# Performance work log

Hardware: AMD Instinct MI355X
Metric: run time of the kernel (lower is better)

## Reference

```python
import jax, jax.numpy as jnp
import numpy as np

EPS = 1e-8

def div_small(a, b):
    b_safe = b * (b > EPS) + (b <= EPS) * EPS
    return a / b_safe

def cos_full(q1h, q2h, w):
    # q1h [b,s1,h], q2h [b,s1_or_1,h], w [P,h] -> [b,s1,P]
    a = q1h[:, :, None, :] * w          # [b,s1,P,h]
    c = q2h[:, :, None, :] * w          # [b,s1|1,P,h]
    num = jnp.sum(a * c, axis=-1)
    den = jnp.maximum(jnp.linalg.norm(a, axis=-1) * jnp.linalg.norm(c, axis=-1), EPS)
    return num / den

def cos_maxpool(q1h, q2h, w):
    # q1h [b,s1,h], q2h [b,s2,h], w [P,h] -> max over s2 of cosine -> [b,s1,P]
    a = q1h[:, :, None, :] * w          # [b,s1,P,h]
    c = q2h[:, :, None, :] * w          # [b,s2,P,h]
    num = jnp.einsum('biph,bjph->bijp', a, c)            # [b,s1,s2,P]
    na = jnp.linalg.norm(a, axis=-1)                     # [b,s1,P]
    nc = jnp.linalg.norm(c, axis=-1)                     # [b,s2,P]
    den = jnp.maximum(na[:, :, None, :] * nc[:, None, :, :], EPS)
    return jnp.max(num / den, axis=2)

def attention(q1, q2):
    # cosine-similarity matrix [b,s1,s2]
    n1 = jnp.linalg.norm(q1, axis=2, keepdims=True)      # [b,s1,1]
    n2 = jnp.linalg.norm(q2, axis=2, keepdims=True)      # [b,s2,1]
    num = jnp.einsum('bih,bjh->bij', q1, q2)
    return div_small(num, n1 * jnp.swapaxes(n2, 1, 2))

def setup_inputs() -> dict:
    key = jax.random.key(0)
    k1, k2, kw = jax.random.split(key, 3)
    q1_batch = jax.random.normal(k1, (16, 128, 512), dtype=jnp.float32)
    q2_batch = jax.random.normal(k2, (16, 128, 512), dtype=jnp.float32)
    W = jax.random.normal(kw, (8, 16, 256), dtype=jnp.float32)
    return {"q1_batch": q1_batch, "q2_batch": q2_batch, "W": W}

def reference(q1_batch, q2_batch, W):
    h = q1_batch.shape[-1] // 2
    q1_fw, q1_bw = q1_batch[..., :h], q1_batch[..., h:]
    q2_fw, q2_bw = q2_batch[..., :h], q2_batch[..., h:]

    # 1) full matching against last (fw) / first (bw) q2 state
    full_fw = cos_full(q1_fw, q2_fw[:, -1:, :], W[0])
    full_bw = cos_full(q1_bw, q2_bw[:, :1, :], W[1])

    # 2) max-pool matching over all q2 positions
    max_fw = cos_maxpool(q1_fw, q2_fw, W[2])
    max_bw = cos_maxpool(q1_bw, q2_bw, W[3])

    # 3) attentive matching
    att_fw = attention(q1_fw, q2_fw)                     # [b,s1,s2]
    att_bw = attention(q1_bw, q2_bw)
    at_q2_fw = att_fw[..., None] * q2_fw[:, None, :, :]  # [b,s1,s2,h]
    at_q2_bw = att_bw[..., None] * q2_bw[:, None, :, :]
    mean_fw = div_small(at_q2_fw.sum(axis=2), att_fw.sum(axis=2, keepdims=True))
    # NOTE: denominator intentionally uses att_fw (bug preserved from source)
    mean_bw = div_small(at_q2_bw.sum(axis=2), att_fw.sum(axis=2, keepdims=True))
    attn_fw = cos_full(q1_fw, mean_fw, W[4])
    attn_bw = cos_full(q1_bw, mean_bw, W[5])

    # 4) max-attentive matching
    max_at_fw = at_q2_fw.max(axis=2)                     # [b,s1,h]
    max_at_bw = at_q2_bw.max(axis=2)
    maxattn_fw = cos_full(q1_fw, max_at_fw, W[6])
    maxattn_bw = cos_full(q1_bw, max_at_bw, W[7])

    return jnp.concatenate(
        [full_fw, full_bw, max_fw, max_bw, attn_fw, attn_bw, maxattn_fw, maxattn_bw],
        axis=-1)
```

## Files before the change

kernel.cpp:

```cpp
#include <hip/hip_runtime.h>
#include <hip/hip_bf16.h>

#define B 16
#define L 128
#define H 256
#define H2 512
#define P 16
#define EPSF 1e-8f
#define LDSTR 72

typedef __attribute__((ext_vector_type(8))) short short8;
typedef __attribute__((ext_vector_type(4))) short short4v;
typedef __attribute__((ext_vector_type(4))) float f32x4;

__device__ __forceinline__ short f2bf(float x) {
    unsigned u = __builtin_bit_cast(unsigned, x);
    u += 0x7fffu + ((u >> 16) & 1u);
    return (short)(u >> 16);
}
__device__ __forceinline__ float bf2f(short s) {
    unsigned u = ((unsigned)(unsigned short)s) << 16;
    return __builtin_bit_cast(float, u);
}
__device__ __forceinline__ short8 pack8(float4 x, float4 y) {
    short8 s;
    s[0] = f2bf(x.x); s[1] = f2bf(x.y); s[2] = f2bf(x.z); s[3] = f2bf(x.w);
    s[4] = f2bf(y.x); s[5] = f2bf(y.y); s[6] = f2bf(y.z); s[7] = f2bf(y.w);
    return s;
}
__device__ __forceinline__ float dot4(float4 v) {
    return v.x * v.x + v.y * v.y + v.z * v.z + v.w * v.w;
}
__device__ __forceinline__ float4 mul4(float4 a, float4 b) {
    return make_float4(a.x * b.x, a.y * b.y, a.z * b.z, a.w * b.w);
}

__global__ void __launch_bounds__(64) k_att_v3(
        const float* __restrict__ q1, const float* __restrict__ q2,
        float* __restrict__ att_fw, float* __restrict__ att_bw,
        float* __restrict__ attsum) {
    int bx = blockIdx.x;
    int b = bx >> 1, dir = bx & 1;
    int m0 = blockIdx.y * 16, n0 = blockIdx.z * 16;
    int l = threadIdx.x, q = l >> 4, coll = l & 15;
    size_t bL = (size_t)b * L;

    const float* arow = q1 + (bL + m0 + coll) * H2 + dir * H;
    const float* brow = q2 + (bL + n0 + coll) * H2 + dir * H;

    f32x4 acc = (f32x4){0.f, 0.f, 0.f, 0.f};
    float na = 0.f, nc = 0.f;
#pragma unroll
    for (int ks = 0; ks < 8; ks++) {
        int koff = ks * 32 + q * 8;
        float4 a0 = *(const float4*)(arow + koff);
        float4 a1 = *(const float4*)(arow + koff + 4);
        float4 b0 = *(const float4*)(brow + koff);
        float4 b1 = *(const float4*)(brow + koff + 4);
        na += dot4(a0) + dot4(a1);
        nc += dot4(b0) + dot4(b1);
        short8 af = pack8(a0, a1);
        short8 bf = pack8(b0, b1);
        acc = __builtin_amdgcn_mfma_f32_16x16x32_bf16(af, bf, acc, 0, 0, 0);
    }
    na += __shfl_xor(na, 16); na += __shfl_xor(na, 32);
    nc += __shfl_xor(nc, 16); nc += __shfl_xor(nc, 32);
    float na_s = sqrtf(na), nc_s = sqrtf(nc);

    float* attout = dir ? att_bw : att_fw;
    float rsum[4];
#pragma unroll
    for (int r = 0; r < 4; r++) {
        float nar = __shfl(na_s, (l & 48) + q * 4 + r);
        float den = nar * nc_s;
        den = den > EPSF ? den : EPSF;
        float a = acc[r] / den;
        attout[(bL + m0 + q * 4 + r) * L + n0 + coll] = a;
        rsum[r] = a;
    }
    if (dir == 0) {
#pragma unroll
        for (int off = 1; off < 16; off <<= 1)
#pragma unroll
            for (int r = 0; r < 4; r++)
                rsum[r] += __shfl_xor(rsum[r], off, 16);
        if (coll == 0)
#pragma unroll
            for (int r = 0; r < 4; r++)
                atomicAdd(&attsum[bL + m0 + q * 4 + r], rsum[r]);
    }
}

__global__ void __launch_bounds__(256) k_meanmax_v3(
        const float* __restrict__ q2,
        const float* __restrict__ att_fw, const float* __restrict__ att_bw,
        const float* __restrict__ attsum,
        float* __restrict__ mean_fw, float* __restrict__ mean_bw,
        float* __restrict__ maxat_fw, float* __restrict__ maxat_bw) {
    int bd = blockIdx.x;
    int b = bd >> 1, dir = bd & 1;
    int i0 = blockIdx.y * 4;
    int t = threadIdx.x;
    int wave = t >> 6, l = t & 63;
    size_t bL = (size_t)b * L;

    __shared__ float at[4][L];
    __shared__ float Ss[4];
    __shared__ f32x4 red[4][64][4];

    const float* att = dir ? att_bw : att_fw;
    for (int v = t; v < 4 * L; v += 256)
        at[v >> 7][v & 127] = att[(bL + i0 + (v >> 7)) * L + (v & 127)];
    if (t < 4) {
        float s = attsum[bL + i0 + t];
        Ss[t] = s > EPSF ? s : EPSF;
    }
    __syncthreads();

    f32x4 sum[4], mx[4];
#pragma unroll
    for (int r = 0; r < 4; r++) {
        sum[r] = (f32x4){0.f, 0.f, 0.f, 0.f};
        mx[r] = (f32x4){-INFINITY, -INFINITY, -INFINITY, -INFINITY};
    }
    const float* q2b = q2 + bL * H2 + dir * H;
    for (int jj = 0; jj < 32; jj++) {
        int j = wave * 32 + jj;
        float4 c = *(const float4*)(q2b + (size_t)j * H2 + l * 4);
#pragma unroll
        for (int r = 0; r < 4; r++) {
            float w = at[r][j];
            f32x4 v = { w * c.x, w * c.y, w * c.z, w * c.w };
            sum[r] += v;
            mx[r][0] = fmaxf(mx[r][0], v[0]);
            mx[r][1] = fmaxf(mx[r][1], v[1]);
            mx[r][2] = fmaxf(mx[r][2], v[2]);
            mx[r][3] = fmaxf(mx[r][3], v[3]);
        }
    }
    float* meanout = dir ? mean_bw : mean_fw;
    float* maxout = dir ? maxat_bw : maxat_fw;
    for (int rr = 0; rr < 2; rr++) {
        __syncthreads();
        red[wave][l][0] = sum[rr * 2];
        red[wave][l][1] = mx[rr * 2];
        red[wave][l][2] = sum[rr * 2 + 1];
        red[wave][l][3] = mx[rr * 2 + 1];
        __syncthreads();
        if (t < 128) {
            int r2 = t >> 6;
            int lane = t & 63;
            f32x4 s = red[0][lane][r2 * 2];
            f32x4 m = red[0][lane][r2 * 2 + 1];
            for (int w = 1; w < 4; w++) {
                s += red[w][lane][r2 * 2];
                f32x4 m2 = red[w][lane][r2 * 2 + 1];
                m[0] = fmaxf(m[0], m2[0]);
                m[1] = fmaxf(m[1], m2[1]);
                m[2] = fmaxf(m[2], m2[2]);
                m[3] = fmaxf(m[3], m2[3]);
            }
            int row = i0 + rr * 2 + r2;
            float inv = 1.f / Ss[rr * 2 + r2];
            size_t o = (bL + row) * H + lane * 4;
            *(f32x4*)(meanout + o) = s * inv;
            *(f32x4*)(maxout + o) = m;
        }
    }
}

__global__ void __launch_bounds__(256) k_cosfull_v3(
        const float* __restrict__ q1, const float* __restrict__ q2,
        const float* __restrict__ mean_fw, const float* __restrict__ mean_bw,
        const float* __restrict__ maxat_fw, const float* __restrict__ maxat_bw,
        const float* __restrict__ W, float* __restrict__ out) {
    int bg = blockIdx.x;
    int b = bg >> 4;
    int i0 = (bg & 15) * 8;
    int piece = blockIdx.y;
    int t = threadIdx.x;
    int p = t >> 4, l = t & 15;
    size_t bL = (size_t)b * L;

    int widx, colb, dir, cstride;
    const float* cptr;
    switch (piece) {
        case 0: widx = 0; colb = 0;   dir = 0; cptr = q2 + (bL + L - 1) * H2;  cstride = 0; break;
        case 1: widx = 1; colb = 16;  dir = 1; cptr = q2 + bL * H2 + H;        cstride = 0; break;
        case 2: widx = 4; colb = 64;  dir = 0; cptr = mean_fw + bL * H;        cstride = H; break;
        case 3: widx = 5; colb = 80;  dir = 1; cptr = mean_bw + bL * H;        cstride = H; break;
        case 4: widx = 6; colb = 96;  dir = 0; cptr = maxat_fw + bL * H;       cstride = H; break;
        default: widx = 7; colb = 112; dir = 1; cptr = maxat_bw + bL * H;      cstride = H; break;
    }
    const float* wrow = W + ((size_t)widx * P + p) * H;
    float wsq[16];
#pragma unroll
    for (int k = 0; k < 16; k++) {
        float wv = wrow[l + 16 * k];
        wsq[k] = wv * wv;
    }
    for (int ii = 0; ii < 8; ii++) {
        int i = i0 + ii;
        const float* r1 = q1 + (bL + i) * H2 + dir * H;
        const float* crow = cptr + (size_t)i * cstride;
        float num = 0, na = 0, nc = 0;
#pragma unroll
        for (int k = 0; k < 16; k++) {
            int h = l + 16 * k;
            float a = r1[h];
            float c = crow[h];
            num += a * c * wsq[k];
            na  += a * a * wsq[k];
            nc  += c * c * wsq[k];
        }
        for (int off = 8; off; off >>= 1) {
            num += __shfl_down(num, off, 16);
            na  += __shfl_down(na,  off, 16);
            nc  += __shfl_down(nc,  off, 16);
        }
        if (l == 0) {
            float den = sqrtf(na) * sqrtf(nc);
            den = den > EPSF ? den : EPSF;
            out[(bL + i) * 128 + colb + p] = num / den;
        }
    }
}

__global__ void __launch_bounds__(256) k_maxpool_v2(
        const float* __restrict__ q1, const float* __restrict__ q2,
        const float* __restrict__ W, float* __restrict__ out) {
    int bd = blockIdx.x;
    int b = bd >> 1, dir = bd & 1;
    int p = blockIdx.y;
    int t = threadIdx.x;
    int wave = t >> 6, l = t & 63;
    int q = l >> 4, coll = l & 15;
    int m0 = blockIdx.z * 64 + wave * 16;
    size_t bL = (size_t)b * L;

    __shared__ short Bs[128 * LDSTR];
    __shared__ float wf[H];
    __shared__ float ncs[128];

    if (t < 64)
        *(float4*)(wf + t * 4) =
            *(const float4*)(W + ((size_t)(2 + dir) * P + p) * H + t * 4);
    __syncthreads();

    f32x4 acc[8];
#pragma unroll
    for (int nt = 0; nt < 8; nt++) acc[nt] = (f32x4){0.f, 0.f, 0.f, 0.f};
    float ncp = 0.f, nap = 0.f;

    int brow = t >> 1, bc0 = (t & 1) * 32;
    const float* q1b = q1 + bL * H2 + dir * H;
    const float* q2b = q2 + bL * H2 + dir * H;
    const float* arow = q1b + (size_t)(m0 + coll) * H2;
    const float* brp = q2b + (size_t)brow * H2;

    for (int kt = 0; kt < 4; kt++) {
        int k0 = kt * 64;
#pragma unroll
        for (int cc = 0; cc < 8; cc++) {
            float4 v = *(const float4*)(brp + k0 + bc0 + cc * 4);
            float4 wv4 = *(const float4*)(wf + k0 + bc0 + cc * 4);
            float4 x = mul4(v, wv4);
            short4v s = { f2bf(x.x), f2bf(x.y), f2bf(x.z), f2bf(x.w) };
            *(short4v*)(Bs + brow * LDSTR + bc0 + cc * 4) = s;
            float f0 = bf2f(s[0]), f1 = bf2f(s[1]), f2v = bf2f(s[2]), f3 = bf2f(s[3]);
            ncp += f0 * f0 + f1 * f1 + f2v * f2v + f3 * f3;
        }
        __syncthreads();
#pragma unroll
        for (int ks = 0; ks < 2; ks++) {
            int koff = ks * 32 + q * 8;
            float4 a0 = *(const float4*)(arow + k0 + koff);
            float4 a1 = *(const float4*)(arow + k0 + koff + 4);
            float4 w0 = *(const float4*)(wf + k0 + koff);
            float4 w1 = *(const float4*)(wf + k0 + koff + 4);
            float4 e0 = mul4(a0, w0), e1 = mul4(a1, w1);
            short8 af = pack8(e0, e1);
#pragma unroll
            for (int j = 0; j < 8; j++) {
                float f = bf2f(af[j]);
                nap += f * f;
            }
#pragma unroll
            for (int nt = 0; nt < 8; nt++) {
                short8 bf = *(const short8*)(Bs + (nt * 16 + coll) * LDSTR + koff);
                acc[nt] = __builtin_amdgcn_mfma_f32_16x16x32_bf16(af, bf, acc[nt], 0, 0, 0);
            }
        }
        __syncthreads();
    }
    ncp += __shfl_xor(ncp, 1);
    if ((t & 1) == 0) ncs[brow] = sqrtf(ncp);
    nap += __shfl_xor(nap, 16);
    nap += __shfl_xor(nap, 32);
    float na_s = sqrtf(nap);
    __syncthreads();

    float nar[4];
#pragma unroll
    for (int r = 0; r < 4; r++)
        nar[r] = __shfl(na_s, (l & 48) + q * 4 + r);
    float rmax[4] = {-INFINITY, -INFINITY, -INFINITY, -INFINITY};
#pragma unroll
    for (int nt = 0; nt < 8; nt++) {
        float ncv = ncs[nt * 16 + coll];
#pragma unroll
        for (int r = 0; r < 4; r++) {
            float den = fmaxf(nar[r] * ncv, EPSF);
            rmax[r] = fmaxf(rmax[r], acc[nt][r] / den);
        }
    }
#pragma unroll
    for (int off = 1; off < 16; off <<= 1)
#pragma unroll
        for (int r = 0; r < 4; r++)
            rmax[r] = fmaxf(rmax[r], __shfl_xor(rmax[r], off, 16));
    if (coll == 0)
#pragma unroll
        for (int r = 0; r < 4; r++)
            out[(bL + m0 + q * 4 + r) * 128 + 32 + dir * 16 + p] = rmax[r];
}

extern "C" void kernel_launch(void* const* d_in, const int* in_sizes, int n_in,
                              void* d_out, int out_size, void* d_ws, size_t ws_size,
                              hipStream_t stream) {
    const float* q1 = (const float*)d_in[0];
    const float* q2 = (const float*)d_in[1];
    const float* W  = (const float*)d_in[2];
    float* out = (float*)d_out;

    float* ws = (float*)d_ws;
    float* attsum = ws;
    float* att_fw = attsum + B * L;
    float* att_bw = att_fw + (size_t)B * L * L;
    float* mean_fw = att_bw + (size_t)B * L * L;
    float* mean_bw = mean_fw + (size_t)B * L * H;
    float* maxat_fw = mean_bw + (size_t)B * L * H;
    float* maxat_bw = maxat_fw + (size_t)B * L * H;

    hipMemsetAsync(attsum, 0, B * L * sizeof(float), stream);
    k_maxpool_v2<<<dim3(B * 2, P, 2), 256, 0, stream>>>(q1, q2, W, out);
    k_att_v3<<<dim3(B * 2, 8, 8), 64, 0, stream>>>(q1, q2, att_fw, att_bw, attsum);
    k_meanmax_v3<<<dim3(B * 2, 32), 256, 0, stream>>>(q2, att_fw, att_bw, attsum,
                                                      mean_fw, mean_bw, maxat_fw, maxat_bw);
    k_cosfull_v3<<<dim3(B * 16, 6), 256, 0, stream>>>(q1, q2, mean_fw, mean_bw,
                                                      maxat_fw, maxat_bw, W, out);
}
```

Measured before the change: 132.9 us.

## Add prep kernel for bf16 inputs and norms, restructure att and maxpool kernels

Adds a prep kernel that converts q1/q2 to bf16 and precomputes row norms and per-perspective weighted norms, so the attention and maxpool kernels no longer recompute them. The attention kernel now stages a 16-row A tile and all 128 B rows in LDS, with four waves per block. It reduces the row sums in shared memory and writes them directly instead of using atomics. The maxpool kernel loads the full K range into LDS once instead of looping over K tiles, and cosfull uses vectorized float4 loads. The cost is an extra launch, which redundantly computes weighted norms for 16 perspectives per row, plus extra workspace traffic.

```diff
diff --git a/kernel.cpp b/kernel.cpp
--- a/kernel.cpp
+++ b/kernel.cpp
@@ -7,7 +7,7 @@
 #define H2 512
 #define P 16
 #define EPSF 1e-8f
-#define LDSTR 72
+#define LDSTR2 264
 
 typedef __attribute__((ext_vector_type(8))) short short8;
 typedef __attribute__((ext_vector_type(4))) short short4v;
@@ -35,48 +35,119 @@
     return make_float4(a.x * b.x, a.y * b.y, a.z * b.z, a.w * b.w);
 }
 
-__global__ void __launch_bounds__(64) k_att_v3(
+__global__ void __launch_bounds__(64) k_prep(
         const float* __restrict__ q1, const float* __restrict__ q2,
+        const float* __restrict__ W,
+        short* __restrict__ q1b, short* __restrict__ q2b,
+        float* __restrict__ nex,
+        float* __restrict__ nW) {
+    int row = blockIdx.x;
+    int src = blockIdx.y;
+    int l = threadIdx.x;
+    const float* base = (src ? q2 : q1) + (size_t)row * H2;
+    short* qb = (src ? q2b : q1b) + (size_t)row * H2;
+
+    float4 xf = *(const float4*)(base + l * 4);
+    float4 xb = *(const float4*)(base + H + l * 4);
+    short4v sf = { f2bf(xf.x), f2bf(xf.y), f2bf(xf.z), f2bf(xf.w) };
+    short4v sb = { f2bf(xb.x), f2bf(xb.y), f2bf(xb.z), f2bf(xb.w) };
+    *(short4v*)(qb + l * 4) = sf;
+    *(short4v*)(qb + H + l * 4) = sb;
+
+    float nf = dot4(xf), nb = dot4(xb);
+#pragma unroll
+    for (int off = 1; off < 64; off <<= 1) {
+        nf += __shfl_xor(nf, off);
+        nb += __shfl_xor(nb, off);
+    }
+    if (l == 0) {
+        nex[(src * 2 + 0) * 2048 + row] = sqrtf(nf);
+        nex[(src * 2 + 1) * 2048 + row] = sqrtf(nb);
+    }
+#pragma unroll
+    for (int dir = 0; dir < 2; dir++) {
+        float4 x = dir ? xb : xf;
+#pragma unroll
+        for (int p = 0; p < P; p++) {
+            float4 w4 = *(const float4*)(W + ((size_t)(2 + dir) * P + p) * H + l * 4);
+            float4 e = mul4(x, w4);
+            float v0 = bf2f(f2bf(e.x)), v1 = bf2f(f2bf(e.y));
+            float v2 = bf2f(f2bf(e.z)), v3 = bf2f(f2bf(e.w));
+            float s = v0 * v0 + v1 * v1 + v2 * v2 + v3 * v3;
+#pragma unroll
+            for (int off = 1; off < 64; off <<= 1) s += __shfl_xor(s, off);
+            if (l == 0)
+                nW[(((size_t)src * 2 + dir) * P + p) * 2048 + row] = sqrtf(s);
+        }
+    }
+}
+
+__global__ void __launch_bounds__(256, 2) k_att_v4(
+        const short* __restrict__ q1b, const short* __restrict__ q2b,
+        const float* __restrict__ nex,
         float* __restrict__ att_fw, float* __restrict__ att_bw,
         float* __restrict__ attsum) {
-    int bx = blockIdx.x;
-    int b = bx >> 1, dir = bx & 1;
-    int m0 = blockIdx.y * 16, n0 = blockIdx.z * 16;
-    int l = threadIdx.x, q = l >> 4, coll = l & 15;
+    int bd = blockIdx.x;
+    int b = bd >> 1, dir = bd & 1;
+    int m0 = blockIdx.y * 16;
+    int t = threadIdx.x;
+    int wave = t >> 6, l = t & 63;
+    int q = l >> 4, coll = l & 15;
+    int n0 = wave * 32;
     size_t bL = (size_t)b * L;
 
-    const float* arow = q1 + (bL + m0 + coll) * H2 + dir * H;
-    const float* brow = q2 + (bL + n0 + coll) * H2 + dir * H;
-
-    f32x4 acc = (f32x4){0.f, 0.f, 0.f, 0.f};
-    float na = 0.f, nc = 0.f;
+    __shared__ short As[16 * LDSTR2];
+    __shared__ short Bs[128 * LDSTR2];
+    __shared__ float part[4][16];
+
+    int rsub = l >> 5, c8 = (l & 31) * 8;
+#pragma unroll
+    for (int j = 0; j < 2; j++) {
+        int r16 = wave * 4 + j * 2 + rsub;
+        short8 v = *(const short8*)(q1b + (bL + m0 + r16) * H2 + dir * H + c8);
+        *(short8*)(As + r16 * LDSTR2 + c8) = v;
+    }
+#pragma unroll
+    for (int j = 0; j < 16; j++) {
+        int r = wave * 32 + j * 2 + rsub;
+        short8 v = *(const short8*)(q2b + (bL + r) * H2 + dir * H + c8);
+        *(short8*)(Bs + r * LDSTR2 + c8) = v;
+    }
+    __syncthreads();
+
+    f32x4 acc[2];
+    acc[0] = (f32x4){0.f, 0.f, 0.f, 0.f};
+    acc[1] = (f32x4){0.f, 0.f, 0.f, 0.f};
 #pragma unroll
     for (int ks = 0; ks < 8; ks++) {
         int koff = ks * 32 + q * 8;
-        float4 a0 = *(const float4*)(arow + koff);
-        float4 a1 = *(const float4*)(arow + koff + 4);
-        float4 b0 = *(const float4*)(brow + koff);
-        float4 b1 = *(const float4*)(brow + koff + 4);
-        na += dot4(a0) + dot4(a1);
-        nc += dot4(b0) + dot4(b1);
-        short8 af = pack8(a0, a1);
-        short8 bf = pack8(b0, b1);
-        acc = __builtin_amdgcn_mfma_f32_16x16x32_bf16(af, bf, acc, 0, 0, 0);
-    }
-    na += __shfl_xor(na, 16); na += __shfl_xor(na, 32);
-    nc += __shfl_xor(nc, 16); nc += __shfl_xor(nc, 32);
-    float na_s = sqrtf(na), nc_s = sqrtf(nc);
+        short8 af = *(const short8*)(As + coll * LDSTR2 + koff);
+        short8 b0 = *(const short8*)(Bs + (n0 + coll) * LDSTR2 + koff);
+        short8 b1 = *(const short8*)(Bs + (n0 + 16 + coll) * LDSTR2 + koff);
+        acc[0] = __builtin_amdgcn_mfma_f32_16x16x32_bf16(af, b0, acc[0], 0, 0, 0);
+        acc[1] = __builtin_amdgcn_mfma_f32_16x16x32_bf16(af, b1, acc[1], 0, 0, 0);
+    }
+
+    const float* n1a = nex + (size_t)dir * 2048 + bL;
+    const float* n2a = nex + (size_t)(2 + dir) * 2048 + bL;
+    float n1v[4];
+#pragma unroll
+    for (int r = 0; r < 4; r++) n1v[r] = n1a[m0 + q * 4 + r];
 
     float* attout = dir ? att_bw : att_fw;
-    float rsum[4];
-#pragma unroll
-    for (int r = 0; r < 4; r++) {
-        float nar = __shfl(na_s, (l & 48) + q * 4 + r);
-        float den = nar * nc_s;
-        den = den > EPSF ? den : EPSF;
-        float a = acc[r] / den;
-        attout[(bL + m0 + q * 4 + r) * L + n0 + coll] = a;
-        rsum[r] = a;
+    float rsum[4] = {0.f, 0.f, 0.f, 0.f};
+#pragma unroll
+    for (int nt = 0; nt < 2; nt++) {
+        int col = n0 + nt * 16 + coll;
+        float n2v = n2a[col];
+#pragma unroll
+        for (int r = 0; r < 4; r++) {
+            float den = n1v[r] * n2v;
+            den = den > EPSF ? den : EPSF;
+            float a = acc[nt][r] / den;
+            attout[(bL + m0 + q * 4 + r) * L + col] = a;
+            rsum[r] += a;
+        }
     }
     if (dir == 0) {
 #pragma unroll
@@ -87,7 +158,10 @@
         if (coll == 0)
 #pragma unroll
             for (int r = 0; r < 4; r++)
-                atomicAdd(&attsum[bL + m0 + q * 4 + r], rsum[r]);
+                part[wave][q * 4 + r] = rsum[r];
+        __syncthreads();
+        if (t < 16)
+            attsum[bL + m0 + t] = part[0][t] + part[1][t] + part[2][t] + part[3][t];
     }
 }
 
@@ -169,7 +243,7 @@
     }
 }
 
-__global__ void __launch_bounds__(256) k_cosfull_v3(
+__global__ void __launch_bounds__(256) k_cosfull_v4(
         const float* __restrict__ q1, const float* __restrict__ q2,
         const float* __restrict__ mean_fw, const float* __restrict__ mean_bw,
         const float* __restrict__ maxat_fw, const float* __restrict__ maxat_bw,
@@ -192,26 +266,28 @@
         case 4: widx = 6; colb = 96;  dir = 0; cptr = maxat_fw + bL * H;       cstride = H; break;
         default: widx = 7; colb = 112; dir = 1; cptr = maxat_bw + bL * H;      cstride = H; break;
     }
-    const float* wrow = W + ((size_t)widx * P + p) * H;
-    float wsq[16];
-#pragma unroll
-    for (int k = 0; k < 16; k++) {
-        float wv = wrow[l + 16 * k];
-        wsq[k] = wv * wv;
+    const float* wrow = W + ((size_t)widx * P + p) * H + l * 16;
+    float4 wq[4];
+#pragma unroll
+    for (int c = 0; c < 4; c++) {
+        float4 w4 = *(const float4*)(wrow + c * 4);
+        wq[c] = mul4(w4, w4);
     }
     for (int ii = 0; ii < 8; ii++) {
         int i = i0 + ii;
-        const float* r1 = q1 + (bL + i) * H2 + dir * H;
-        const float* crow = cptr + (size_t)i * cstride;
+        const float* r1 = q1 + (bL + i) * H2 + dir * H + l * 16;
+        const float* crow = cptr + (size_t)i * cstride + l * 16;
         float num = 0, na = 0, nc = 0;
 #pragma unroll
-        for (int k = 0; k < 16; k++) {
-            int h = l + 16 * k;
-            float a = r1[h];
-            float c = crow[h];
-            num += a * c * wsq[k];
-            na  += a * a * wsq[k];
-            nc  += c * c * wsq[k];
+        for (int c = 0; c < 4; c++) {
+            float4 a = *(const float4*)(r1 + c * 4);
+            float4 cc = *(const float4*)(crow + c * 4);
+            num += a.x * cc.x * wq[c].x + a.y * cc.y * wq[c].y
+                 + a.z * cc.z * wq[c].z + a.w * cc.w * wq[c].w;
+            na  += a.x * a.x * wq[c].x + a.y * a.y * wq[c].y
+                 + a.z * a.z * wq[c].z + a.w * a.w * wq[c].w;
+            nc  += cc.x * cc.x * wq[c].x + cc.y * cc.y * wq[c].y
+                 + cc.z * cc.z * wq[c].z + cc.w * cc.w * wq[c].w;
         }
         for (int off = 8; off; off >>= 1) {
             num += __shfl_down(num, off, 16);
@@ -226,9 +302,10 @@
     }
 }
 
-__global__ void __launch_bounds__(256) k_maxpool_v2(
+__global__ void __launch_bounds__(256, 2) k_maxpool_v4(
         const float* __restrict__ q1, const float* __restrict__ q2,
-        const float* __restrict__ W, float* __restrict__ out) {
+        const float* __restrict__ W, const float* __restrict__ nW,
+        float* __restrict__ out) {
     int bd = blockIdx.x;
     int b = bd >> 1, dir = bd & 1;
     int p = blockIdx.y;
@@ -238,76 +315,54 @@
     int m0 = blockIdx.z * 64 + wave * 16;
     size_t bL = (size_t)b * L;
 
-    __shared__ short Bs[128 * LDSTR];
+    __shared__ short Bs[128 * LDSTR2];
     __shared__ float wf[H];
-    __shared__ float ncs[128];
-
+
+    const float* wbase = W + ((size_t)(2 + dir) * P + p) * H;
     if (t < 64)
-        *(float4*)(wf + t * 4) =
-            *(const float4*)(W + ((size_t)(2 + dir) * P + p) * H + t * 4);
+        *(float4*)(wf + t * 4) = *(const float4*)(wbase + t * 4);
+
+    float4 wreg = *(const float4*)(wbase + l * 4);
+    const float* q2b = q2 + bL * H2 + dir * H;
+#pragma unroll 8
+    for (int j = 0; j < 32; j++) {
+        int r = wave * 32 + j;
+        float4 v = *(const float4*)(q2b + (size_t)r * H2 + l * 4);
+        float4 e = mul4(v, wreg);
+        short4v s = { f2bf(e.x), f2bf(e.y), f2bf(e.z), f2bf(e.w) };
+        *(short4v*)(Bs + r * LDSTR2 + l * 4) = s;
+    }
     __syncthreads();
 
     f32x4 acc[8];
 #pragma unroll
     for (int nt = 0; nt < 8; nt++) acc[nt] = (f32x4){0.f, 0.f, 0.f, 0.f};
-    float ncp = 0.f, nap = 0.f;
-
-    int brow = t >> 1, bc0 = (t & 1) * 32;
-    const float* q1b = q1 + bL * H2 + dir * H;
-    const float* q2b = q2 + bL * H2 + dir * H;
-    const float* arow = q1b + (size_t)(m0 + coll) * H2;
-    const float* brp = q2b + (size_t)brow * H2;
-
-    for (int kt = 0; kt < 4; kt++) {
-        int k0 = kt * 64;
-#pragma unroll
-        for (int cc = 0; cc < 8; cc++) {
-            float4 v = *(const float4*)(brp + k0 + bc0 + cc * 4);
-            float4 wv4 = *(const float4*)(wf + k0 + bc0 + cc * 4);
-            float4 x = mul4(v, wv4);
-            short4v s = { f2bf(x.x), f2bf(x.y), f2bf(x.z), f2bf(x.w) };
-            *(short4v*)(Bs + brow * LDSTR + bc0 + cc * 4) = s;
-            float f0 = bf2f(s[0]), f1 = bf2f(s[1]), f2v = bf2f(s[2]), f3 = bf2f(s[3]);
-            ncp += f0 * f0 + f1 * f1 + f2v * f2v + f3 * f3;
-        }
-        __syncthreads();
-#pragma unroll
-        for (int ks = 0; ks < 2; ks++) {
-            int koff = ks * 32 + q * 8;
-            float4 a0 = *(const float4*)(arow + k0 + koff);
-            float4 a1 = *(const float4*)(arow + k0 + koff + 4);
-            float4 w0 = *(const float4*)(wf + k0 + koff);
-            float4 w1 = *(const float4*)(wf + k0 + koff + 4);
-            float4 e0 = mul4(a0, w0), e1 = mul4(a1, w1);
-            short8 af = pack8(e0, e1);
-#pragma unroll
-            for (int j = 0; j < 8; j++) {
-                float f = bf2f(af[j]);
-                nap += f * f;
-            }
-#pragma unroll
-            for (int nt = 0; nt < 8; nt++) {
-                short8 bf = *(const short8*)(Bs + (nt * 16 + coll) * LDSTR + koff);
-                acc[nt] = __builtin_amdgcn_mfma_f32_16x16x32_bf16(af, bf, acc[nt], 0, 0, 0);
-            }
-        }
-        __syncthreads();
-    }
-    ncp += __shfl_xor(ncp, 1);
-    if ((t & 1) == 0) ncs[brow] = sqrtf(ncp);
-    nap += __shfl_xor(nap, 16);
-    nap += __shfl_xor(nap, 32);
-    float na_s = sqrtf(nap);
-    __syncthreads();
-
+
+    const float* arow = q1 + (bL + m0 + coll) * H2 + dir * H;
+#pragma unroll
+    for (int ks = 0; ks < 8; ks++) {
+        int koff = ks * 32 + q * 8;
+        float4 a0 = *(const float4*)(arow + koff);
+        float4 a1 = *(const float4*)(arow + koff + 4);
+        float4 w0 = *(const float4*)(wf + koff);
+        float4 w1 = *(const float4*)(wf + koff + 4);
+        short8 af = pack8(mul4(a0, w0), mul4(a1, w1));
+#pragma unroll
+        for (int nt = 0; nt < 8; nt++) {
+            short8 bf = *(const short8*)(Bs + (nt * 16 + coll) * LDSTR2 + koff);
+            acc[nt] = __builtin_amdgcn_mfma_f32_16x16x32_bf16(af, bf, acc[nt], 0, 0, 0);
+        }
+    }
+
+    const float* naW = nW + (((size_t)0 * 2 + dir) * P + p) * 2048 + bL;
+    const float* ncW = nW + (((size_t)1 * 2 + dir) * P + p) * 2048 + bL;
     float nar[4];
 #pragma unroll
-    for (int r = 0; r < 4; r++)
-        nar[r] = __shfl(na_s, (l & 48) + q * 4 + r);
+    for (int r = 0; r < 4; r++) nar[r] = naW[m0 + q * 4 + r];
     float rmax[4] = {-INFINITY, -INFINITY, -INFINITY, -INFINITY};
 #pragma unroll
     for (int nt = 0; nt < 8; nt++) {
-        float ncv = ncs[nt * 16 + coll];
+        float ncv = ncW[nt * 16 + coll];
 #pragma unroll
         for (int r = 0; r < 4; r++) {
             float den = fmaxf(nar[r] * ncv, EPSF);
@@ -335,18 +390,23 @@
 
     float* ws = (float*)d_ws;
     float* attsum = ws;
-    float* att_fw = attsum + B * L;
+    float* att_fw = attsum + 2048;
     float* att_bw = att_fw + (size_t)B * L * L;
     float* mean_fw = att_bw + (size_t)B * L * L;
     float* mean_bw = mean_fw + (size_t)B * L * H;
     float* maxat_fw = mean_bw + (size_t)B * L * H;
     float* maxat_bw = maxat_fw + (size_t)B * L * H;
-
-    hipMemsetAsync(attsum, 0, B * L * sizeof(float), stream);
-    k_maxpool_v2<<<dim3(B * 2, P, 2), 256, 0, stream>>>(q1, q2, W, out);
-    k_att_v3<<<dim3(B * 2, 8, 8), 64, 0, stream>>>(q1, q2, att_fw, att_bw, attsum);
+    float* nex = maxat_bw + (size_t)B * L * H;
+    float* nW  = nex + 4 * 2048;
+    short* q1b = (short*)(nW + (size_t)2 * 2 * P * 2048);
+    short* q2b = q1b + (size_t)2048 * H2;
+
+    hipMemsetAsync(attsum, 0, 2048 * sizeof(float), stream);
+    k_prep<<<dim3(2048, 2), 64, 0, stream>>>(q1, q2, W, q1b, q2b, nex, nW);
+    k_maxpool_v4<<<dim3(B * 2, P, 2), 256, 0, stream>>>(q1, q2, W, nW, out);
+    k_att_v4<<<dim3(B * 2, 8), 256, 0, stream>>>(q1b, q2b, nex, att_fw, att_bw, attsum);
     k_meanmax_v3<<<dim3(B * 2, 32), 256, 0, stream>>>(q2, att_fw, att_bw, attsum,
                                                       mean_fw, mean_bw, maxat_fw, maxat_bw);
-    k_cosfull_v3<<<dim3(B * 16, 6), 256, 0, stream>>>(q1, q2, mean_fw, mean_bw,
+    k_cosfull_v4<<<dim3(B * 16, 6), 256, 0, stream>>>(q1, q2, mean_fw, mean_bw,
                                                       maxat_fw, maxat_bw, W, out);
 }
```

Measured after the change: 146.0 us. +9.8%, slower.
